# Performance work log

Hardware: AMD Instinct MI355X
Metric: run time of the kernel (lower is better)

## Reference

```python
import jax, jax.numpy as jnp
import numpy as np

MARGIN = 1.0  # init kwarg margin
EPS = 1e-16


def setup_inputs() -> dict:
    key = jax.random.key(0)
    k1, k2 = jax.random.split(key)
    embeddings = jax.random.normal(k1, (512, 128), dtype=jnp.float32)
    labels = jax.random.randint(k2, (512,), 0, 32)
    return {"embeddings": embeddings, "labels": labels}


def _pairwise_l2(e):
    # exact p=2 cdist via explicit differences; safe sqrt so grad at d=0 is 0
    diff = e[:, None, :] - e[None, :, :]          # [N, N, D]
    sq = jnp.sum(diff * diff, axis=-1)             # [N, N]
    safe = jnp.where(sq > 0, sq, 1.0)
    return jnp.where(sq > 0, jnp.sqrt(safe), 0.0)


def reference(embeddings, labels):
    # _batch_all_triplet_loss (default mining_type='online_hard_negative')
    n = labels.shape[0]
    d = _pairwise_l2(embeddings)                   # [N, N]

    not_eye = ~jnp.eye(n, dtype=bool)
    # distinct (i, j, k) triplets
    distinct = not_eye[:, :, None] & not_eye[:, None, :] & not_eye[None, :, :]
    label_eq = labels[:, None] == labels[None, :]  # symmetric [N, N]
    # labels[i] == labels[j] and labels[i] != labels[k]
    mask = label_eq[:, :, None] & (~label_eq[:, None, :]) & distinct  # [N, N, N]

    # d(a, p) - d(a, n) + margin, masked and hinged
    triplet_loss = mask.astype(d.dtype) * (d[:, :, None] - d[:, None, :] + MARGIN)
    triplet_loss = jnp.maximum(triplet_loss, 0.0)

    n_positive = jnp.sum(triplet_loss > EPS).astype(d.dtype)
    n_triplets = jnp.sum(mask).astype(d.dtype)
    fraction_positive = n_positive / (n_triplets + EPS)
    loss = jnp.sum(triplet_loss) / (n_positive + EPS)
    return loss, fraction_positive
```

## Files before the change

kernel.cpp:

```cpp
#include <hip/hip_runtime.h>

constexpr int N = 512;
constexpr int D = 128;
constexpr float MARGIN = 1.0f;
constexpr float EPS_T = 1e-16f;

__global__ __launch_bounds__(512) void triplet_main_k(
    const float* __restrict__ emb, const int* __restrict__ labels,
    double* __restrict__ partial)
{
    __shared__ float  ei[D];
    __shared__ float  drow[N];
    __shared__ float  posd[N];
    __shared__ int    npos_s;
    __shared__ double red[24];

    const int i    = blockIdx.x;
    const int tid  = threadIdx.x;
    const int lane = tid & 63;
    const int wid  = tid >> 6;

    if (tid < D) ei[tid] = emb[(size_t)i * D + tid];
    const int lk = labels[tid];
    const int li = labels[i];
    __syncthreads();

    const float4* ea  = reinterpret_cast<const float4*>(ei);
    const int     sub = tid & 7;
    #pragma unroll
    for (int p = 0; p < 8; ++p) {
        const int r = p * 64 + (tid >> 3);
        const float4* er = reinterpret_cast<const float4*>(emb + (size_t)r * D);
        float sq = 0.f;
        #pragma unroll
        for (int c = 0; c < 4; ++c) {
            const int idx = sub + 8 * c;
            float4 v = er[idx];
            float4 a = ea[idx];
            float d0 = a.x - v.x, d1 = a.y - v.y;
            float d2 = a.z - v.z, d3 = a.w - v.w;
            sq += d0 * d0 + d1 * d1 + d2 * d2 + d3 * d3;
        }
        sq += __shfl_xor(sq, 1);
        sq += __shfl_xor(sq, 2);
        sq += __shfl_xor(sq, 4);
        if (sub == 0) drow[r] = (sq > 0.f) ? sqrtf(sq) : 0.f;
    }
    __syncthreads();

    if (wid == 0) {
        int base = 0;
        #pragma unroll
        for (int r = 0; r < 8; ++r) {
            const int j = r * 64 + lane;
            const bool pred = (labels[j] == li) && (j != i);
            const unsigned long long m = __ballot(pred);
            if (pred) posd[base + __popcll(m & ((1ull << lane) - 1ull))] = drow[j];
            base += __popcll(m);
        }
        if (lane == 0) npos_s = base;
    }
    __syncthreads();

    const int   npos = npos_s;
    const float dik  = drow[tid];
    double sum = 0.0;
    int np_i = 0, nt_i = 0;
    if (lk != li) {
        #pragma unroll 4
        for (int p = 0; p < npos; ++p) {
            const float t = (posd[p] - dik) + MARGIN;
            if (t > EPS_T) { sum += (double)t; ++np_i; }
        }
        nt_i = npos;
    }

    double s = sum, p = (double)np_i, t = (double)nt_i;
    #pragma unroll
    for (int off = 32; off > 0; off >>= 1) {
        s += __shfl_down(s, off);
        p += __shfl_down(p, off);
        t += __shfl_down(t, off);
    }
    if (lane == 0) { red[wid] = s; red[8 + wid] = p; red[16 + wid] = t; }
    __syncthreads();
    if (tid == 0) {
        double S = 0.0, P = 0.0, T = 0.0;
        #pragma unroll
        for (int w = 0; w < 8; ++w) { S += red[w]; P += red[8 + w]; T += red[16 + w]; }
        partial[i]         = S;
        partial[N + i]     = P;
        partial[2 * N + i] = T;
    }
}

__global__ __launch_bounds__(512) void triplet_final_k(
    const double* __restrict__ partial, float* __restrict__ out)
{
    __shared__ double red[24];
    const int tid  = threadIdx.x;
    const int lane = tid & 63;
    const int wid  = tid >> 6;
    double a = partial[tid];
    double b = partial[N + tid];
    double c = partial[2 * N + tid];
    #pragma unroll
    for (int off = 32; off > 0; off >>= 1) {
        a += __shfl_down(a, off);
        b += __shfl_down(b, off);
        c += __shfl_down(c, off);
    }
    if (lane == 0) { red[wid] = a; red[8 + wid] = b; red[16 + wid] = c; }
    __syncthreads();
    if (tid == 0) {
        double S = 0.0, P = 0.0, T = 0.0;
        #pragma unroll
        for (int w = 0; w < 8; ++w) { S += red[w]; P += red[8 + w]; T += red[16 + w]; }
        out[0] = (float)(S / (P + 1e-16));
        out[1] = (float)(P / (T + 1e-16));
    }
}

extern "C" void kernel_launch(void* const* d_in, const int* in_sizes, int n_in,
                              void* d_out, int out_size, void* d_ws, size_t ws_size,
                              hipStream_t stream) {
    const float* emb   = (const float*)d_in[0];
    const int*   lab   = (const int*)d_in[1];
    float*       out   = (float*)d_out;
    double*      parts = (double*)d_ws;

    triplet_main_k<<<N, 512, 0, stream>>>(emb, lab, parts);
    triplet_final_k<<<1, 512, 0, stream>>>(parts, out);
}
```

Baseline: 16.03 us.

## Process four anchors per block to reuse embedding row loads

Each block now handles four anchor rows instead of one, loading each comparison embedding row once and computing distances against all four anchors. The grid shrinks from 512 to 128 blocks and the final reduction is resized to match. This cuts redundant global loads of the embedding matrix and per-block launch overhead. In exchange there are fewer blocks to spread across compute units, and more serial work per thread in the triplet loop.

```diff
diff --git a/kernel.cpp b/kernel.cpp
--- a/kernel.cpp
+++ b/kernel.cpp
@@ -2,6 +2,8 @@
 
 constexpr int N = 512;
 constexpr int D = 128;
+constexpr int A = 4;
+constexpr int NBLK = N / A;
 constexpr float MARGIN = 1.0f;
 constexpr float EPS_T = 1e-16f;
 
@@ -9,70 +11,82 @@
     const float* __restrict__ emb, const int* __restrict__ labels,
     double* __restrict__ partial)
 {
-    __shared__ float  ei[D];
-    __shared__ float  drow[N];
-    __shared__ float  posd[N];
-    __shared__ int    npos_s;
+    __shared__ float  ei[A][D];
+    __shared__ float  drow[A][N];
+    __shared__ float  posd[A][N];
+    __shared__ int    npos_s[A];
     __shared__ double red[24];
 
-    const int i    = blockIdx.x;
+    const int i0   = blockIdx.x * A;
     const int tid  = threadIdx.x;
     const int lane = tid & 63;
     const int wid  = tid >> 6;
 
-    if (tid < D) ei[tid] = emb[(size_t)i * D + tid];
+    ei[tid >> 7][tid & (D - 1)] = emb[(size_t)i0 * D + tid];
     const int lk = labels[tid];
-    const int li = labels[i];
+    int liA[A];
+    #pragma unroll
+    for (int a = 0; a < A; ++a) liA[a] = labels[i0 + a];
     __syncthreads();
 
-    const float4* ea  = reinterpret_cast<const float4*>(ei);
-    const int     sub = tid & 7;
-    #pragma unroll
+    const int sub = tid & 7;
+    #pragma unroll 2
     for (int p = 0; p < 8; ++p) {
         const int r = p * 64 + (tid >> 3);
         const float4* er = reinterpret_cast<const float4*>(emb + (size_t)r * D);
-        float sq = 0.f;
+        float4 v[4];
         #pragma unroll
-        for (int c = 0; c < 4; ++c) {
-            const int idx = sub + 8 * c;
-            float4 v = er[idx];
-            float4 a = ea[idx];
-            float d0 = a.x - v.x, d1 = a.y - v.y;
-            float d2 = a.z - v.z, d3 = a.w - v.w;
-            sq += d0 * d0 + d1 * d1 + d2 * d2 + d3 * d3;
+        for (int c = 0; c < 4; ++c) v[c] = er[sub + 8 * c];
+        #pragma unroll
+        for (int a = 0; a < A; ++a) {
+            const float4* ea = reinterpret_cast<const float4*>(ei[a]);
+            float sq = 0.f;
+            #pragma unroll
+            for (int c = 0; c < 4; ++c) {
+                const float4 w = ea[sub + 8 * c];
+                float d0 = w.x - v[c].x, d1 = w.y - v[c].y;
+                float d2 = w.z - v[c].z, d3 = w.w - v[c].w;
+                sq += d0 * d0 + d1 * d1 + d2 * d2 + d3 * d3;
+            }
+            sq += __shfl_xor(sq, 1);
+            sq += __shfl_xor(sq, 2);
+            sq += __shfl_xor(sq, 4);
+            if (sub == 0) drow[a][r] = (sq > 0.f) ? sqrtf(sq) : 0.f;
         }
-        sq += __shfl_xor(sq, 1);
-        sq += __shfl_xor(sq, 2);
-        sq += __shfl_xor(sq, 4);
-        if (sub == 0) drow[r] = (sq > 0.f) ? sqrtf(sq) : 0.f;
     }
     __syncthreads();
 
-    if (wid == 0) {
+    if (wid < A) {
+        const int ia = i0 + wid;
+        const int li = liA[wid];
         int base = 0;
         #pragma unroll
         for (int r = 0; r < 8; ++r) {
             const int j = r * 64 + lane;
-            const bool pred = (labels[j] == li) && (j != i);
+            const bool pred = (labels[j] == li) && (j != ia);
             const unsigned long long m = __ballot(pred);
-            if (pred) posd[base + __popcll(m & ((1ull << lane) - 1ull))] = drow[j];
+            if (pred) posd[wid][base + __popcll(m & ((1ull << lane) - 1ull))] = drow[wid][j];
             base += __popcll(m);
         }
-        if (lane == 0) npos_s = base;
+        if (lane == 0) npos_s[wid] = base;
     }
     __syncthreads();
 
-    const int   npos = npos_s;
-    const float dik  = drow[tid];
     double sum = 0.0;
     int np_i = 0, nt_i = 0;
-    if (lk != li) {
-        #pragma unroll 4
-        for (int p = 0; p < npos; ++p) {
-            const float t = (posd[p] - dik) + MARGIN;
-            if (t > EPS_T) { sum += (double)t; ++np_i; }
+    #pragma unroll
+    for (int a = 0; a < A; ++a) {
+        const int li = liA[a];
+        if (lk != li) {
+            const float dik  = drow[a][tid];
+            const int   npos = npos_s[a];
+            #pragma unroll 4
+            for (int p = 0; p < npos; ++p) {
+                const float t = (posd[a][p] - dik) + MARGIN;
+                if (t > EPS_T) { sum += (double)t; ++np_i; }
+            }
+            nt_i += npos;
         }
-        nt_i = npos;
     }
 
     double s = sum, p = (double)np_i, t = (double)nt_i;
@@ -88,34 +102,34 @@
         double S = 0.0, P = 0.0, T = 0.0;
         #pragma unroll
         for (int w = 0; w < 8; ++w) { S += red[w]; P += red[8 + w]; T += red[16 + w]; }
-        partial[i]         = S;
-        partial[N + i]     = P;
-        partial[2 * N + i] = T;
+        partial[blockIdx.x]            = S;
+        partial[NBLK + blockIdx.x]     = P;
+        partial[2 * NBLK + blockIdx.x] = T;
     }
 }
 
-__global__ __launch_bounds__(512) void triplet_final_k(
+__global__ __launch_bounds__(128) void triplet_final_k(
     const double* __restrict__ partial, float* __restrict__ out)
 {
-    __shared__ double red[24];
+    __shared__ double red[6];
     const int tid  = threadIdx.x;
     const int lane = tid & 63;
     const int wid  = tid >> 6;
     double a = partial[tid];
-    double b = partial[N + tid];
-    double c = partial[2 * N + tid];
+    double b = partial[NBLK + tid];
+    double c = partial[2 * NBLK + tid];
     #pragma unroll
     for (int off = 32; off > 0; off >>= 1) {
         a += __shfl_down(a, off);
         b += __shfl_down(b, off);
         c += __shfl_down(c, off);
     }
-    if (lane == 0) { red[wid] = a; red[8 + wid] = b; red[16 + wid] = c; }
+    if (lane == 0) { red[wid] = a; red[2 + wid] = b; red[4 + wid] = c; }
     __syncthreads();
     if (tid == 0) {
-        double S = 0.0, P = 0.0, T = 0.0;
-        #pragma unroll
-        for (int w = 0; w < 8; ++w) { S += red[w]; P += red[8 + w]; T += red[16 + w]; }
+        const double S = red[0] + red[1];
+        const double P = red[2] + red[3];
+        const double T = red[4] + red[5];
         out[0] = (float)(S / (P + 1e-16));
         out[1] = (float)(P / (T + 1e-16));
     }
@@ -129,6 +143,6 @@
     float*       out   = (float*)d_out;
     double*      parts = (double*)d_ws;
 
-    triplet_main_k<<<N, 512, 0, stream>>>(emb, lab, parts);
-    triplet_final_k<<<1, 512, 0, stream>>>(parts, out);
+    triplet_main_k<<<NBLK, 512, 0, stream>>>(emb, lab, parts);
+    triplet_final_k<<<1, 128, 0, stream>>>(parts, out);
 }
```

New measurement: 22.24 us. 1.39x slower.

## Keep anchor row in registers, parallelize positive compaction, and shrink final reduction

Applied to the files above, without the earlier changes.

The anchor embedding now loads straight into registers instead of staging through shared memory, which drops one barrier. Each loop iteration computes two distance rows to raise memory-level parallelism. Positive-distance compaction now runs on all eight waves using per-wave counts and a prefix sum, instead of a single serial wave. Partials are written interleaved per block and reduced by a single-wave final kernel. The positive buffer shrinks to 128 entries, which assumes small label classes, and a min-blocks launch hint is added.

```diff
diff --git a/kernel.cpp b/kernel.cpp
--- a/kernel.cpp
+++ b/kernel.cpp
@@ -5,13 +5,13 @@
 constexpr float MARGIN = 1.0f;
 constexpr float EPS_T = 1e-16f;
 
-__global__ __launch_bounds__(512) void triplet_main_k(
+__global__ __launch_bounds__(512, 4) void triplet_main_k(
     const float* __restrict__ emb, const int* __restrict__ labels,
     double* __restrict__ partial)
 {
-    __shared__ float  ei[D];
     __shared__ float  drow[N];
-    __shared__ float  posd[N];
+    __shared__ float  posd[128];
+    __shared__ int    cnt[8];
     __shared__ int    npos_s;
     __shared__ double red[24];
 
@@ -19,46 +19,60 @@
     const int tid  = threadIdx.x;
     const int lane = tid & 63;
     const int wid  = tid >> 6;
+    const int sub  = tid & 7;
+    const int grp  = tid >> 3;
 
-    if (tid < D) ei[tid] = emb[(size_t)i * D + tid];
+    const float4* ea = reinterpret_cast<const float4*>(emb + (size_t)i * D);
+    float4 A0[4];
+    #pragma unroll
+    for (int c = 0; c < 4; ++c) A0[c] = ea[sub + 8 * c];
+
     const int lk = labels[tid];
     const int li = labels[i];
-    __syncthreads();
 
-    const float4* ea  = reinterpret_cast<const float4*>(ei);
-    const int     sub = tid & 7;
-    #pragma unroll
-    for (int p = 0; p < 8; ++p) {
-        const int r = p * 64 + (tid >> 3);
-        const float4* er = reinterpret_cast<const float4*>(emb + (size_t)r * D);
-        float sq = 0.f;
+    #pragma unroll 2
+    for (int p = 0; p < 4; ++p) {
+        const int r0 = p * 128 + grp;
+        const int r1 = r0 + 64;
+        const float4* er0 = reinterpret_cast<const float4*>(emb + (size_t)r0 * D);
+        const float4* er1 = reinterpret_cast<const float4*>(emb + (size_t)r1 * D);
+        float4 V0[4], V1[4];
+        #pragma unroll
+        for (int c = 0; c < 4; ++c) { V0[c] = er0[sub + 8 * c]; V1[c] = er1[sub + 8 * c]; }
+        float sq0 = 0.f, sq1 = 0.f;
         #pragma unroll
         for (int c = 0; c < 4; ++c) {
-            const int idx = sub + 8 * c;
-            float4 v = er[idx];
-            float4 a = ea[idx];
-            float d0 = a.x - v.x, d1 = a.y - v.y;
-            float d2 = a.z - v.z, d3 = a.w - v.w;
-            sq += d0 * d0 + d1 * d1 + d2 * d2 + d3 * d3;
+            float d0 = A0[c].x - V0[c].x, d1 = A0[c].y - V0[c].y;
+            float d2 = A0[c].z - V0[c].z, d3 = A0[c].w - V0[c].w;
+            sq0 += d0 * d0 + d1 * d1 + d2 * d2 + d3 * d3;
+            d0 = A0[c].x - V1[c].x; d1 = A0[c].y - V1[c].y;
+            d2 = A0[c].z - V1[c].z; d3 = A0[c].w - V1[c].w;
+            sq1 += d0 * d0 + d1 * d1 + d2 * d2 + d3 * d3;
         }
-        sq += __shfl_xor(sq, 1);
-        sq += __shfl_xor(sq, 2);
-        sq += __shfl_xor(sq, 4);
-        if (sub == 0) drow[r] = (sq > 0.f) ? sqrtf(sq) : 0.f;
+        sq0 += __shfl_xor(sq0, 1); sq1 += __shfl_xor(sq1, 1);
+        sq0 += __shfl_xor(sq0, 2); sq1 += __shfl_xor(sq1, 2);
+        sq0 += __shfl_xor(sq0, 4); sq1 += __shfl_xor(sq1, 4);
+        if (sub == 0) {
+            drow[r0] = (sq0 > 0.f) ? sqrtf(sq0) : 0.f;
+            drow[r1] = (sq1 > 0.f) ? sqrtf(sq1) : 0.f;
+        }
     }
     __syncthreads();
 
-    if (wid == 0) {
-        int base = 0;
+    const int j = tid;
+    const bool pr = (labels[j] == li) && (j != i);
+    const unsigned long long m = __ballot(pr);
+    if (lane == 0) cnt[wid] = __popcll(m);
+    __syncthreads();
+    int base = 0;
+    #pragma unroll
+    for (int w = 0; w < 8; ++w) base += (w < wid) ? cnt[w] : 0;
+    if (pr) posd[base + __popcll(m & ((1ull << lane) - 1ull))] = drow[j];
+    if (tid == 0) {
+        int t = 0;
         #pragma unroll
-        for (int r = 0; r < 8; ++r) {
-            const int j = r * 64 + lane;
-            const bool pred = (labels[j] == li) && (j != i);
-            const unsigned long long m = __ballot(pred);
-            if (pred) posd[base + __popcll(m & ((1ull << lane) - 1ull))] = drow[j];
-            base += __popcll(m);
-        }
-        if (lane == 0) npos_s = base;
+        for (int w = 0; w < 8; ++w) t += cnt[w];
+        npos_s = t;
     }
     __syncthreads();
 
@@ -67,7 +81,6 @@
     double sum = 0.0;
     int np_i = 0, nt_i = 0;
     if (lk != li) {
-        #pragma unroll 4
         for (int p = 0; p < npos; ++p) {
             const float t = (posd[p] - dik) + MARGIN;
             if (t > EPS_T) { sum += (double)t; ++np_i; }
@@ -88,36 +101,32 @@
         double S = 0.0, P = 0.0, T = 0.0;
         #pragma unroll
         for (int w = 0; w < 8; ++w) { S += red[w]; P += red[8 + w]; T += red[16 + w]; }
-        partial[i]         = S;
-        partial[N + i]     = P;
-        partial[2 * N + i] = T;
+        partial[4 * blockIdx.x + 0] = S;
+        partial[4 * blockIdx.x + 1] = P;
+        partial[4 * blockIdx.x + 2] = T;
     }
 }
 
-__global__ __launch_bounds__(512) void triplet_final_k(
+__global__ __launch_bounds__(64) void triplet_final_k(
     const double* __restrict__ partial, float* __restrict__ out)
 {
-    __shared__ double red[24];
-    const int tid  = threadIdx.x;
-    const int lane = tid & 63;
-    const int wid  = tid >> 6;
-    double a = partial[tid];
-    double b = partial[N + tid];
-    double c = partial[2 * N + tid];
+    const int lane = threadIdx.x;
+    double a = 0.0, b = 0.0, c = 0.0;
+    #pragma unroll
+    for (int bk = lane; bk < N; bk += 64) {
+        a += partial[4 * bk + 0];
+        b += partial[4 * bk + 1];
+        c += partial[4 * bk + 2];
+    }
     #pragma unroll
     for (int off = 32; off > 0; off >>= 1) {
         a += __shfl_down(a, off);
         b += __shfl_down(b, off);
         c += __shfl_down(c, off);
     }
-    if (lane == 0) { red[wid] = a; red[8 + wid] = b; red[16 + wid] = c; }
-    __syncthreads();
-    if (tid == 0) {
-        double S = 0.0, P = 0.0, T = 0.0;
-        #pragma unroll
-        for (int w = 0; w < 8; ++w) { S += red[w]; P += red[8 + w]; T += red[16 + w]; }
-        out[0] = (float)(S / (P + 1e-16));
-        out[1] = (float)(P / (T + 1e-16));
+    if (lane == 0) {
+        out[0] = (float)(a / (b + 1e-16));
+        out[1] = (float)(b / (c + 1e-16));
     }
 }
 
@@ -130,5 +139,5 @@
     double*      parts = (double*)d_ws;
 
     triplet_main_k<<<N, 512, 0, stream>>>(emb, lab, parts);
-    triplet_final_k<<<1, 512, 0, stream>>>(parts, out);
+    triplet_final_k<<<1, 64, 0, stream>>>(parts, out);
 }
```

Result: slower. 17.55 us (+9.5%).
